# Kernel optimization log

Measured on AMD Instinct MI355X. Metric: run time of the kernel, lower is better.

## Reference

```python
import jax, jax.numpy as jnp
import numpy as np

DN3D = ('NCDHW', 'OIDHW', 'NCDHW')

def conv_t3d(x, w, stride):
    # PyTorch ConvTranspose3d with padding=0: w is (C_in, C_out, k1,k2,k3).
    # Equivalent dilated conv: flip spatial dims, swap in/out channels,
    # lhs_dilation=stride, padding k-1 on each side.
    wf = jnp.flip(w, axis=(2, 3, 4)).transpose(1, 0, 2, 3, 4)  # (O, I, k, k, k)
    pad = [(k - 1, k - 1) for k in w.shape[2:]]
    dn = jax.lax.conv_dimension_numbers(x.shape, wf.shape, DN3D)
    return jax.lax.conv_general_dilated(x, wf, (1, 1, 1), pad,
                                        lhs_dilation=stride, dimension_numbers=dn)

def conv3d(x, w, stride, pad):
    dn = jax.lax.conv_dimension_numbers(x.shape, w.shape, DN3D)
    return jax.lax.conv_general_dilated(x, w, stride, [(pad, pad)] * 3,
                                        dimension_numbers=dn)

def setup_inputs() -> dict:
    key = jax.random.key(0)
    ks = jax.random.split(key, 7)
    out_ch, emb, p = 4, 256, 8
    B, T, D = 2, 8, 4  # batch, 4th spatial dim, coarse grid (input_size//patch_size)
    s = 0.05
    return {
        'x':  jax.random.normal(ks[0], (B, T, out_ch * emb, D, D, D), jnp.float32),
        'w1': jax.random.normal(ks[1], (out_ch * emb, out_ch * 2, p // 2, p // 2, p // 2), jnp.float32) * s,
        'b1': jax.random.normal(ks[2], (out_ch * 2,), jnp.float32) * s,
        'w2': jax.random.normal(ks[3], (out_ch * 2, out_ch * 2, 4, 4, 4), jnp.float32) * s,
        'b2': jax.random.normal(ks[4], (out_ch * 2,), jnp.float32) * s,
        'w3': jax.random.normal(ks[5], (out_ch, out_ch * 2, 4, 4, 4), jnp.float32) * s,
        'b3': jax.random.normal(ks[6], (out_ch,), jnp.float32) * s,
    }

def reference(x, w1, b1, w2, b2, w3, b3):
    # x: (B, D4, C_in, D1, D2, D3). All 4D kernels are size/stride 1 along D4,
    # so fold D4 into the batch and run 3D (de)convs.
    B, T, C, D, _, _ = x.shape
    h = x.reshape(B * T, C, D, D, D)
    bcast = lambda b: b[None, :, None, None, None]
    h = jnp.tanh(conv_t3d(h, w1, (4, 4, 4)) + bcast(b1))   # -> (BT, 8, 16,16,16)
    h = jnp.tanh(conv_t3d(h, w2, (4, 4, 4)) + bcast(b2))   # -> (BT, 8, 64,64,64)
    h = conv3d(h, w3, (2, 2, 2), 1) + bcast(b3)             # -> (BT, 4, 32,32,32)
    out = h.reshape(B, T, *h.shape[1:])                     # (B, D4, C, 32,32,32)
    return jnp.moveaxis(out, 1, -1)                         # (B, C, 32,32,32, D4)
```

## Files before the change

kernel.cpp:

```cpp
#include <hip/hip_runtime.h>
#include <cstdint>

typedef short bf16x8 __attribute__((ext_vector_type(8)));
typedef float f32x4 __attribute__((ext_vector_type(4)));
typedef _Float16 half2_t __attribute__((ext_vector_type(2)));

__device__ __forceinline__ unsigned short f2bf(float f) {
  unsigned u = __builtin_bit_cast(unsigned, f);
  u += 0x7fffu + ((u >> 16) & 1u);
  return (unsigned short)(u >> 16);
}
__device__ __forceinline__ unsigned pkh2(float a, float b) {
  return __builtin_bit_cast(unsigned, __builtin_amdgcn_cvt_pkrtz(a, b));
}
__device__ __forceinline__ float fast_tanh(float x) {
  float e = __builtin_amdgcn_exp2f(x * 2.885390081777927f);
  return 1.0f - 2.0f * __builtin_amdgcn_rcpf(e + 1.0f);
}

#if __has_builtin(__builtin_amdgcn_fdot2)
__device__ __forceinline__ float dot2h(unsigned a, unsigned b, float c) {
  return __builtin_amdgcn_fdot2(__builtin_bit_cast(half2_t, a),
                                __builtin_bit_cast(half2_t, b), c, false);
}
#else
__device__ __forceinline__ float dot2h(unsigned a, unsigned b, float c) {
  half2_t av = __builtin_bit_cast(half2_t, a);
  half2_t bv = __builtin_bit_cast(half2_t, b);
  c = fmaf((float)av.x, (float)bv.x, c);
  c = fmaf((float)av.y, (float)bv.y, c);
  return c;
}
#endif

template <int ITERS>
__global__ __launch_bounds__(256) void k_stage1(const float* __restrict__ x,
                                                const float* __restrict__ w1,
                                                const float* __restrict__ w3,
                                                float* __restrict__ part,
                                                unsigned* __restrict__ wtab) {
  __shared__ __align__(16) char lds_raw[64 * 65 * 4];
  unsigned short* As = (unsigned short*)lds_raw;
  unsigned short* Bs = (unsigned short*)(lds_raw + 5120);
  float* Cs = (float*)lds_raw;

  const int tid = threadIdx.x;
  if (blockIdx.x == 0) {
    int l = tid << 2;
#pragma unroll
    for (int j = 0; j < 4; ++j) {
      int d = l + j;
      int slot = d & 3, chU = (d >> 2) & 1, kh = (d >> 3) & 3,
          kd = (d >> 5) & 3, cio = d >> 7;
      int co = (chU << 1) + (slot & 1);
      int kwb = (slot >> 1) << 1;
      int base = ((co << 3) + cio) * 64 + (kd << 4) + (kh << 2) + kwb;
      wtab[d] = pkh2(w3[base], w3[base + 1]);
    }
  }

  const int ks = blockIdx.x >> 7;
  const int bt = (blockIdx.x >> 3) & 15;
  const int co = blockIdx.x & 7;
  const int w = tid >> 6, lane = tid & 63, lm = lane & 15, q = lane >> 4;
  const int rrow = tid & 63, kgr = tid >> 6;

  f32x4 acc[4];
#pragma unroll
  for (int i = 0; i < 4; ++i) acc[i] = (f32x4){0.f, 0.f, 0.f, 0.f};

  const float* gA = x + (bt << 16) + ((size_t)(ks * ITERS * 32) << 6);
  const float* gB = w1 + (co << 6) + (size_t)(ks * ITERS * 32) * 512;

  float va[2][8], vb[2][8];
#define S1_LOAD(buf, it)                            \
  {                                                 \
    const int kb = (it) * 32 + (kgr << 3);          \
    _Pragma("unroll") for (int j = 0; j < 8; ++j) { \
      va[buf][j] = gA[((kb + j) << 6) | rrow];      \
      vb[buf][j] = gB[(kb + j) * 512 + rrow];       \
    }                                               \
  }
  S1_LOAD(0, 0);
#pragma unroll
  for (int it = 0; it < ITERS; ++it) {
    const int cur = it & 1;
    if (it + 1 < ITERS) S1_LOAD(cur ^ 1, it + 1);
    uint4 pa, pb;
    pa.x = f2bf(va[cur][0]) | ((unsigned)f2bf(va[cur][1]) << 16);
    pa.y = f2bf(va[cur][2]) | ((unsigned)f2bf(va[cur][3]) << 16);
    pa.z = f2bf(va[cur][4]) | ((unsigned)f2bf(va[cur][5]) << 16);
    pa.w = f2bf(va[cur][6]) | ((unsigned)f2bf(va[cur][7]) << 16);
    pb.x = f2bf(vb[cur][0]) | ((unsigned)f2bf(vb[cur][1]) << 16);
    pb.y = f2bf(vb[cur][2]) | ((unsigned)f2bf(vb[cur][3]) << 16);
    pb.z = f2bf(vb[cur][4]) | ((unsigned)f2bf(vb[cur][5]) << 16);
    pb.w = f2bf(vb[cur][6]) | ((unsigned)f2bf(vb[cur][7]) << 16);
    *(uint4*)&As[rrow * 40 + (kgr << 3)] = pa;
    *(uint4*)&Bs[rrow * 40 + (kgr << 3)] = pb;
    __syncthreads();
    bf16x8 a = *(const bf16x8*)&As[((w << 4) + lm) * 40 + (q << 3)];
#pragma unroll
    for (int nf = 0; nf < 4; ++nf) {
      bf16x8 b = *(const bf16x8*)&Bs[((nf << 4) + lm) * 40 + (q << 3)];
      acc[nf] = __builtin_amdgcn_mfma_f32_16x16x32_bf16(a, b, acc[nf], 0, 0, 0);
    }
    __syncthreads();
  }
#undef S1_LOAD
#pragma unroll
  for (int nf = 0; nf < 4; ++nf)
#pragma unroll
    for (int r = 0; r < 4; ++r) {
      int m = (w << 4) + (q << 2) + r;
      int n = (nf << 4) + lm;
      Cs[m * 65 + n] = acc[nf][r];
    }
  __syncthreads();
  float* dst = part + (((size_t)((ks << 4) + bt)) << 15) + co;
#pragma unroll
  for (int j = 0; j < 16; ++j) {
    int pos = (tid << 4) + j;
    int z = pos >> 8, y = (pos >> 4) & 15, xx = pos & 15;
    int m = ((z >> 2) << 4) + ((y >> 2) << 2) + (xx >> 2);
    int n = ((z & 3) << 4) + ((y & 3) << 2) + (xx & 3);
    dst[pos << 3] = Cs[m * 65 + n];
  }
}

__global__ __launch_bounds__(512) void k_stage23(
    const float* __restrict__ part, const float* __restrict__ w2,
    const float* __restrict__ b2, const float* __restrict__ b3,
    const float* __restrict__ b1, const unsigned* __restrict__ wtab,
    float* __restrict__ out, int nsplit) {
  __shared__ __align__(16) unsigned win_d[2][18 * 34 * 12];
  __shared__ __align__(16) unsigned h1p[6 * 240];
  __shared__ __align__(16) unsigned w2p[8 * 320];

  const int tid = threadIdx.x;
  const int bid = blockIdx.x;
  const int bt = bid >> 5;
  const int tile = bid & 31;
  const int tz = tile >> 3, ty = (tile >> 2) & 1, tx = tile & 3;
  const int Z0 = tz << 3, Y0 = ty << 4, X0 = tx << 3;
  const int Qz0 = (Z0 << 1) - 1, Qy0 = (Y0 << 1) - 1, Qx0 = (X0 << 1) - 1;
  const int Uz0 = (tz << 2) - 1, Uy0 = (ty << 3) - 1, Ux0 = (tx << 2) - 1;

  for (int l = tid; l < 2880; l += 512) {
    int ci = l & 7;
    int sp = l >> 3;
    int ux = sp % 6;
    int t1 = sp / 6;
    int uy = t1 % 10;
    int uz = t1 / 10;
    int gz = Uz0 + uz, gy = Uy0 + uy, gx = Ux0 + ux;
    float v = 0.f;
    if ((unsigned)gz < 16u && (unsigned)gy < 16u && (unsigned)gx < 16u) {
      const float* p =
          part + (((size_t)bt << 12) + (gz << 8) + (gy << 4) + gx) * 8 + ci;
      float s = b1[ci];
      for (int sg = 0; sg < nsplit; ++sg) s += p[(size_t)sg << 19];
      v = fast_tanh(s);
    }
    ((_Float16*)h1p)[uz * 480 + uy * 48 + (ux << 3) + ci] = (_Float16)v;
  }
  for (int l = tid; l < 2048; l += 512) {
    int j = l & 3, kx = (l >> 2) & 3, kzy = (l >> 4) & 15, cio = l >> 8;
    int kpos = (kzy << 2) + kx;
    float w0 = w2[(((j << 1) << 3) + cio) * 64 + kpos];
    float w1v = w2[((((j << 1) + 1) << 3) + cio) * 64 + kpos];
    w2p[cio * 320 + kzy * 20 + (kx << 2) + j] = pkh2(w0, w1v);
  }
  for (int u = tid; u < 1224; u += 512) {
    int wz = u / 68;
    int rem = u - wz * 68;
    int wy = rem >> 1;
    int half = rem & 1;
    int qz = Qz0 + wz, qy = Qy0 + wy;
    if ((unsigned)qz < 64u && (unsigned)qy < 64u) continue;
    uint4 zz;
    zz.x = zz.y = zz.z = zz.w = 0u;
#pragma unroll
    for (int bsel = 0; bsel < 2; ++bsel) {
      unsigned* wrow = win_d[bsel] + (wz * 34 + wy) * 12;
      if (half == 0) {
        *(uint4*)wrow = zz;
      } else {
        *(uint4*)(wrow + 4) = zz;
        wrow[8] = 0u;
      }
    }
  }
  __syncthreads();

  float acc[2][4];
#pragma unroll
  for (int a = 0; a < 2; ++a)
#pragma unroll
    for (int i = 0; i < 4; ++i) acc[a][i] = 0.f;

  const int xh = tid & 1, yq = (tid >> 1) & 15, zq = (tid >> 5) & 7;
  const int chS = __builtin_amdgcn_readfirstlane(tid >> 8);

  for (int cio = 0; cio < 8; ++cio) {
    unsigned* wbuf = win_d[cio & 1];
    const float b2c = b2[cio];
    for (int u = tid; u < 1224; u += 512) {
      int wz = u / 68;
      int rem = u - wz * 68;
      int wy = rem >> 1;
      int half = rem & 1;
      int qz = Qz0 + wz, qy = Qy0 + wy;
      if (!((unsigned)qz < 64u && (unsigned)qy < 64u)) continue;
      unsigned* wrow = wbuf + (wz * 34 + wy) * 12;
      int kz = qz & 3, ky = qy & 3;
      int uzp = (qz >> 2) - Uz0, uyp = (qy >> 2) - Uy0;
      const unsigned* w2b = w2p + cio * 320 + ((kz << 2) + ky) * 20;
      uint4 wv[4];
#pragma unroll
      for (int kx = 0; kx < 4; ++kx) wv[kx] = *(const uint4*)(w2b + (kx << 2));
      const unsigned* h1b = h1p + uzp * 240 + uyp * 24;
#define DOT8(hc, kx)                                            \
  dot2h((hc).w, wv[kx].w,                                       \
        dot2h((hc).z, wv[kx].z,                                 \
              dot2h((hc).y, wv[kx].y, dot2h((hc).x, wv[kx].x, b2c))))
      if (half == 0) {
        uint4 h0 = *(const uint4*)(h1b);
        uint4 h1c = *(const uint4*)(h1b + 4);
        uint4 h2c = *(const uint4*)(h1b + 8);
        float vals[8];
        vals[0] = (Qx0 >= 0) ? fast_tanh(DOT8(h0, 3)) : 0.f;
#pragma unroll
        for (int kx = 0; kx < 4; ++kx) vals[1 + kx] = fast_tanh(DOT8(h1c, kx));
#pragma unroll
        for (int kx = 0; kx < 3; ++kx) vals[5 + kx] = fast_tanh(DOT8(h2c, kx));
        uint4 s0;
        s0.x = pkh2(vals[0], vals[1]);
        s0.y = pkh2(vals[2], vals[3]);
        s0.z = pkh2(vals[4], vals[5]);
        s0.w = pkh2(vals[6], vals[7]);
        *(uint4*)wrow = s0;
      } else {
        uint4 h2c = *(const uint4*)(h1b + 8);
        uint4 h3 = *(const uint4*)(h1b + 12);
        uint4 h4 = *(const uint4*)(h1b + 16);
        uint4 h5 = *(const uint4*)(h1b + 20);
        float vals[10];
        vals[0] = fast_tanh(DOT8(h2c, 3));
#pragma unroll
        for (int kx = 0; kx < 4; ++kx) vals[1 + kx] = fast_tanh(DOT8(h3, kx));
#pragma unroll
        for (int kx = 0; kx < 4; ++kx) vals[5 + kx] = fast_tanh(DOT8(h4, kx));
        vals[9] = (Qx0 + 17 < 64) ? fast_tanh(DOT8(h5, 0)) : 0.f;
        uint4 s1;
        s1.x = pkh2(vals[0], vals[1]);
        s1.y = pkh2(vals[2], vals[3]);
        s1.z = pkh2(vals[4], vals[5]);
        s1.w = pkh2(vals[6], vals[7]);
        *(uint4*)(wrow + 4) = s1;
        wrow[8] = pkh2(vals[8], vals[9]);
      }
#undef DOT8
    }
    __syncthreads();
#pragma unroll
    for (int kd = 0; kd < 4; ++kd) {
      int wz = (zq << 1) + kd;
#pragma unroll
      for (int kh = 0; kh < 4; ++kh) {
        int wy = (yq << 1) + kh;
        const unsigned* rowp = wbuf + (wz * 34 + wy) * 12 + (xh << 2);
        uint4 rv = *(const uint4*)rowp;
        unsigned r4 = rowp[4];
        unsigned r[5] = {rv.x, rv.y, rv.z, rv.w, r4};
        const uint4 wv =
            *(const uint4*)&wtab[((((cio << 4) + (kd << 2) + kh) << 1) + chS)
                                 << 2];
        unsigned wA[2] = {wv.x, wv.y};
        unsigned wB[2] = {wv.z, wv.w};
#pragma unroll
        for (int cc = 0; cc < 2; ++cc) {
#pragma unroll
          for (int i = 0; i < 4; ++i) {
            float a0 = dot2h(r[i], wA[cc], acc[cc][i]);
            acc[cc][i] = dot2h(r[i + 1], wB[cc], a0);
          }
        }
      }
    }
  }
  const int ch = tid >> 8;
  const int b = bt >> 3, t8 = bt & 7;
  const int z = Z0 + zq;
  const int y = Y0 + yq;
#pragma unroll
  for (int cc = 0; cc < 2; ++cc) {
    int c4 = (ch << 1) + cc;
    float bias = b3[c4];
#pragma unroll
    for (int i = 0; i < 4; ++i) {
      int xx = X0 + (xh << 2) + i;
      out[(((((b << 2) + c4) * 32 + z) * 32 + y) * 32 + xx) << 3 | t8] =
          acc[cc][i] + bias;
    }
  }
}

extern "C" void kernel_launch(void* const* d_in, const int* in_sizes, int n_in,
                              void* d_out, int out_size, void* d_ws,
                              size_t ws_size, hipStream_t stream) {
  (void)in_sizes; (void)n_in; (void)out_size;
  const float* x = (const float*)d_in[0];
  const float* w1 = (const float*)d_in[1];
  const float* b1 = (const float*)d_in[2];
  const float* w2 = (const float*)d_in[3];
  const float* b2 = (const float*)d_in[4];
  const float* w3 = (const float*)d_in[5];
  const float* b3 = (const float*)d_in[6];
  float* out = (float*)d_out;
  float* part = (float*)d_ws;

  const size_t plane = (size_t)16 * 8 * 4096;
  int nsplit = (ws_size >= 2 * plane * 4 + 4096) ? 2 : 1;
  unsigned* wtab = (unsigned*)(part + (size_t)nsplit * plane);

  if (nsplit == 2)
    k_stage1<16><<<dim3(256), dim3(256), 0, stream>>>(x, w1, w3, part, wtab);
  else
    k_stage1<32><<<dim3(128), dim3(256), 0, stream>>>(x, w1, w3, part, wtab);
  k_stage23<<<dim3(512), dim3(512), 0, stream>>>(part, w2, b2, b3, b1, wtab,
                                                 out, nsplit);
}
```

Measured before the change: 150.7 us.

## Deepen split-K in stage1, switch to fp16 MFMA, and use channel-major partials

Stage1 now splits K up to 8 ways when workspace allows, launching up to 1024 blocks of 4 iterations each instead of 256, and reorders the block index so the split index varies fastest. The bf16 rounding is replaced by packed fp16 conversion feeding the f16 MFMA. Partial results are stored channel-major with float4 writes instead of strided scalar stores, and stage23 reads them in the matching layout. More splits raise the partial traffic and the reduction loop length in stage23, and fp16 conversion without range handling could overflow on large inputs.

New measurement: 154.8 us. 2.7% more time.

```diff
diff --git a/kernel.cpp b/kernel.cpp
--- a/kernel.cpp
+++ b/kernel.cpp
@@ -1,15 +1,10 @@
 #include <hip/hip_runtime.h>
 #include <cstdint>
 
-typedef short bf16x8 __attribute__((ext_vector_type(8)));
+typedef _Float16 f16x8 __attribute__((ext_vector_type(8)));
 typedef float f32x4 __attribute__((ext_vector_type(4)));
 typedef _Float16 half2_t __attribute__((ext_vector_type(2)));
 
-__device__ __forceinline__ unsigned short f2bf(float f) {
-  unsigned u = __builtin_bit_cast(unsigned, f);
-  u += 0x7fffu + ((u >> 16) & 1u);
-  return (unsigned short)(u >> 16);
-}
 __device__ __forceinline__ unsigned pkh2(float a, float b) {
   return __builtin_bit_cast(unsigned, __builtin_amdgcn_cvt_pkrtz(a, b));
 }
@@ -34,11 +29,13 @@
 #endif
 
 template <int ITERS>
-__global__ __launch_bounds__(256) void k_stage1(const float* __restrict__ x,
-                                                const float* __restrict__ w1,
-                                                const float* __restrict__ w3,
-                                                float* __restrict__ part,
-                                                unsigned* __restrict__ wtab) {
+__global__ __launch_bounds__(256, 4) void k_stage1(const float* __restrict__ x,
+                                                   const float* __restrict__ w1,
+                                                   const float* __restrict__ w3,
+                                                   float* __restrict__ part,
+                                                   unsigned* __restrict__ wtab) {
+  constexpr int NS = 32 / ITERS;
+  constexpr int KSB = (NS == 8) ? 3 : (NS == 4) ? 2 : (NS == 2) ? 1 : 0;
   __shared__ __align__(16) char lds_raw[64 * 65 * 4];
   unsigned short* As = (unsigned short*)lds_raw;
   unsigned short* Bs = (unsigned short*)(lds_raw + 5120);
@@ -59,9 +56,9 @@
     }
   }
 
-  const int ks = blockIdx.x >> 7;
-  const int bt = (blockIdx.x >> 3) & 15;
-  const int co = blockIdx.x & 7;
+  const int ks = blockIdx.x & (NS - 1);
+  const int bt = (blockIdx.x >> KSB) & 15;
+  const int co = blockIdx.x >> (KSB + 4);
   const int w = tid >> 6, lane = tid & 63, lm = lane & 15, q = lane >> 4;
   const int rrow = tid & 63, kgr = tid >> 6;
 
@@ -87,22 +84,22 @@
     const int cur = it & 1;
     if (it + 1 < ITERS) S1_LOAD(cur ^ 1, it + 1);
     uint4 pa, pb;
-    pa.x = f2bf(va[cur][0]) | ((unsigned)f2bf(va[cur][1]) << 16);
-    pa.y = f2bf(va[cur][2]) | ((unsigned)f2bf(va[cur][3]) << 16);
-    pa.z = f2bf(va[cur][4]) | ((unsigned)f2bf(va[cur][5]) << 16);
-    pa.w = f2bf(va[cur][6]) | ((unsigned)f2bf(va[cur][7]) << 16);
-    pb.x = f2bf(vb[cur][0]) | ((unsigned)f2bf(vb[cur][1]) << 16);
-    pb.y = f2bf(vb[cur][2]) | ((unsigned)f2bf(vb[cur][3]) << 16);
-    pb.z = f2bf(vb[cur][4]) | ((unsigned)f2bf(vb[cur][5]) << 16);
-    pb.w = f2bf(vb[cur][6]) | ((unsigned)f2bf(vb[cur][7]) << 16);
+    pa.x = pkh2(va[cur][0], va[cur][1]);
+    pa.y = pkh2(va[cur][2], va[cur][3]);
+    pa.z = pkh2(va[cur][4], va[cur][5]);
+    pa.w = pkh2(va[cur][6], va[cur][7]);
+    pb.x = pkh2(vb[cur][0], vb[cur][1]);
+    pb.y = pkh2(vb[cur][2], vb[cur][3]);
+    pb.z = pkh2(vb[cur][4], vb[cur][5]);
+    pb.w = pkh2(vb[cur][6], vb[cur][7]);
     *(uint4*)&As[rrow * 40 + (kgr << 3)] = pa;
     *(uint4*)&Bs[rrow * 40 + (kgr << 3)] = pb;
     __syncthreads();
-    bf16x8 a = *(const bf16x8*)&As[((w << 4) + lm) * 40 + (q << 3)];
+    f16x8 a = *(const f16x8*)&As[((w << 4) + lm) * 40 + (q << 3)];
 #pragma unroll
     for (int nf = 0; nf < 4; ++nf) {
-      bf16x8 b = *(const bf16x8*)&Bs[((nf << 4) + lm) * 40 + (q << 3)];
-      acc[nf] = __builtin_amdgcn_mfma_f32_16x16x32_bf16(a, b, acc[nf], 0, 0, 0);
+      f16x8 b = *(const f16x8*)&Bs[((nf << 4) + lm) * 40 + (q << 3)];
+      acc[nf] = __builtin_amdgcn_mfma_f32_16x16x32_f16(a, b, acc[nf], 0, 0, 0);
     }
     __syncthreads();
   }
@@ -116,14 +113,19 @@
       Cs[m * 65 + n] = acc[nf][r];
     }
   __syncthreads();
-  float* dst = part + (((size_t)((ks << 4) + bt)) << 15) + co;
-#pragma unroll
-  for (int j = 0; j < 16; ++j) {
-    int pos = (tid << 4) + j;
+  float* dst = part + (((size_t)(((ks << 4) + bt) << 3) + co) << 12);
+#pragma unroll
+  for (int j = 0; j < 4; ++j) {
+    int pos = (tid << 2) + (j << 10);
     int z = pos >> 8, y = (pos >> 4) & 15, xx = pos & 15;
     int m = ((z >> 2) << 4) + ((y >> 2) << 2) + (xx >> 2);
-    int n = ((z & 3) << 4) + ((y & 3) << 2) + (xx & 3);
-    dst[pos << 3] = Cs[m * 65 + n];
+    int n = ((z & 3) << 4) + ((y & 3) << 2);
+    float4 v;
+    v.x = Cs[m * 65 + n + 0];
+    v.y = Cs[m * 65 + n + 1];
+    v.z = Cs[m * 65 + n + 2];
+    v.w = Cs[m * 65 + n + 3];
+    *(float4*)&dst[pos] = v;
   }
 }
 
@@ -146,8 +148,8 @@
   const int Uz0 = (tz << 2) - 1, Uy0 = (ty << 3) - 1, Ux0 = (tx << 2) - 1;
 
   for (int l = tid; l < 2880; l += 512) {
-    int ci = l & 7;
-    int sp = l >> 3;
+    int ci = l / 360;
+    int sp = l - ci * 360;
     int ux = sp % 6;
     int t1 = sp / 6;
     int uy = t1 % 10;
@@ -156,7 +158,7 @@
     float v = 0.f;
     if ((unsigned)gz < 16u && (unsigned)gy < 16u && (unsigned)gx < 16u) {
       const float* p =
-          part + (((size_t)bt << 12) + (gz << 8) + (gy << 4) + gx) * 8 + ci;
+          part + (((size_t)(bt << 3) + ci) << 12) + (gz << 8) + (gy << 4) + gx;
       float s = b1[ci];
       for (int sg = 0; sg < nsplit; ++sg) s += p[(size_t)sg << 19];
       v = fast_tanh(s);
@@ -320,13 +322,29 @@
   float* part = (float*)d_ws;
 
   const size_t plane = (size_t)16 * 8 * 4096;
-  int nsplit = (ws_size >= 2 * plane * 4 + 4096) ? 2 : 1;
+  int nsplit = 1;
+  if (ws_size >= 8 * plane * 4 + 4096)
+    nsplit = 8;
+  else if (ws_size >= 4 * plane * 4 + 4096)
+    nsplit = 4;
+  else if (ws_size >= 2 * plane * 4 + 4096)
+    nsplit = 2;
   unsigned* wtab = (unsigned*)(part + (size_t)nsplit * plane);
 
-  if (nsplit == 2)
-    k_stage1<16><<<dim3(256), dim3(256), 0, stream>>>(x, w1, w3, part, wtab);
-  else
-    k_stage1<32><<<dim3(128), dim3(256), 0, stream>>>(x, w1, w3, part, wtab);
+  switch (nsplit) {
+    case 8:
+      k_stage1<4><<<dim3(1024), dim3(256), 0, stream>>>(x, w1, w3, part, wtab);
+      break;
+    case 4:
+      k_stage1<8><<<dim3(512), dim3(256), 0, stream>>>(x, w1, w3, part, wtab);
+      break;
+    case 2:
+      k_stage1<16><<<dim3(256), dim3(256), 0, stream>>>(x, w1, w3, part, wtab);
+      break;
+    default:
+      k_stage1<32><<<dim3(128), dim3(256), 0, stream>>>(x, w1, w3, part, wtab);
+      break;
+  }
   k_stage23<<<dim3(512), dim3(512), 0, stream>>>(part, w2, b2, b3, b1, wtab,
                                                  out, nsplit);
 }
```
